# Kernel tuning notes

Hardware: AMD Instinct MI355X
Metric: run time of the kernel (lower is better)

Reference implementation:

```python
import jax, jax.numpy as jnp
import numpy as np
import math

H, W = 128, 128
FOV_X = 60.0
OPACITY_SCALE = 1.0
T_STOP = 1e-3  # early-termination threshold from the source (transmittance.max() < 0.001)
N_GAUSS = 2048


def setup_inputs() -> dict:
    key = jax.random.key(0)
    ks = jax.random.split(key, 6)
    N = N_GAUSS
    # place Gaussians in front of the camera so they rasterize (view_matrix = identity)
    xy = jax.random.uniform(ks[0], (N, 2), minval=-1.5, maxval=1.5, dtype=jnp.float32)
    z = jax.random.uniform(ks[1], (N, 1), minval=2.0, maxval=6.0, dtype=jnp.float32)
    positions = jnp.concatenate([xy, z], axis=1)
    scales = jax.random.uniform(ks[2], (N, 3), minval=0.02, maxval=0.08, dtype=jnp.float32)
    rotations = jax.random.normal(ks[3], (N, 4), dtype=jnp.float32)
    colors = jax.random.uniform(ks[4], (N, 3), dtype=jnp.float32)
    opacities = jax.random.uniform(ks[5], (N,), dtype=jnp.float32) * 0.9
    view_matrix = jnp.eye(4, dtype=jnp.float32)
    return {"positions": positions, "scales": scales, "rotations": rotations,
            "colors": colors, "opacities": opacities, "view_matrix": view_matrix}


def _preprocess(positions, scales, rotations, view_matrix):
    # quaternion (w,x,y,z) -> rotation matrix, same entry layout as the torch source
    q = rotations / (jnp.linalg.norm(rotations, axis=1, keepdims=True) + 1e-8)
    w, x, y, z = q[:, 0], q[:, 1], q[:, 2], q[:, 3]
    r00 = 1 - 2 * (y * y + z * z); r01 = 2 * (x * y + z * w); r02 = 2 * (x * z - y * w)
    r10 = 2 * (x * y - z * w); r11 = 1 - 2 * (x * x + z * z); r12 = 2 * (y * z + x * w)
    r20 = 2 * (x * z + y * w); r21 = 2 * (y * z - x * w); r22 = 1 - 2 * (x * x + y * y)
    Rm = jnp.stack([jnp.stack([r00, r01, r02], -1),
                    jnp.stack([r10, r11, r12], -1),
                    jnp.stack([r20, r21, r22], -1)], 1)  # (N,3,3)
    s2 = jnp.maximum(scales, 1e-6) ** 2
    # cov3d[i,k] = sum_j R[i,j] * s2[j] * R[k,j]
    cov3d = jnp.einsum('nij,nj,nkj->nik', Rm, s2, Rm)

    Rv = view_matrix[:3, :3]; tv = view_matrix[:3, 3]
    pos_cam = positions @ Rv.T + tv[None, :]
    X, Y, Z = pos_cam[:, 0], pos_cam[:, 1], pos_cam[:, 2]
    depths = Z
    valid = (Z > 0.1).astype(jnp.float32)

    fx = W / 2 / math.tan(math.radians(FOV_X) / 2)
    fy = fx
    Zs = jnp.maximum(Z, 1e-6)
    means_2d = jnp.stack([fx * X / Zs + W / 2, fy * Y / Zs + H / 2], 1)

    # projection Jacobian rows (N,3)
    invZ2 = 1.0 / Zs ** 2
    zeros = jnp.zeros_like(Zs)
    J0 = jnp.stack([fx / Zs, zeros, -fx * X * invZ2], 1)
    J1 = jnp.stack([zeros, fy / Zs, -fy * Y * invZ2], 1)
    SRt0 = jnp.einsum('nij,j->ni', cov3d, Rv[0])
    SRt1 = jnp.einsum('nij,j->ni', cov3d, Rv[1])
    c00 = jnp.sum(J0 * SRt0, 1)
    c01 = jnp.sum(J0 * SRt1, 1)
    c11 = jnp.sum(J1 * SRt1, 1)

    # radii from eigenvalue BEFORE the 1e-6 eye regularization (as in source)
    tr = c00 + c11
    det = c00 * c11 - c01 ** 2
    disc = jnp.maximum(tr ** 2 - 4 * det, 0.0)
    lam = (tr + jnp.sqrt(disc)) / 2.0
    radii = 3.0 * jnp.sqrt(jnp.maximum(lam, 1e-8))
    c00 = c00 + 1e-6
    c11 = c11 + 1e-6
    return means_2d, c00, c01, c11, depths, radii, valid


def _render(means_2d, c00, c01, c11, colors, opacities, depths, radii):
    # depth sort descending, exactly as torch.argsort(depths, descending=True)
    order = jnp.argsort(-depths)
    mu = means_2d[order]; col = colors[order]; op = opacities[order]; r = radii[order]
    c00 = c00[order]; c01 = c01[order]; c11 = c11[order]
    det = c00 * c11 - c01 ** 2 + 1e-8
    ic00 = (c11 / det)[:, None, None]
    ic01 = (-c01 / det)[:, None, None]
    ic11 = (c00 / det)[:, None, None]

    px = jnp.arange(W, dtype=jnp.float32)[None, None, :]   # (1,1,W)
    py = jnp.arange(H, dtype=jnp.float32)[None, :, None]   # (1,H,1)
    mux = mu[:, 0][:, None, None]; muy = mu[:, 1][:, None, None]
    rb = r[:, None, None]
    # bbox via int() truncation semantics of the source
    px_min = jnp.maximum(0.0, jnp.trunc(mux - rb)); px_max = jnp.minimum(float(W), jnp.trunc(mux + rb) + 1)
    py_min = jnp.maximum(0.0, jnp.trunc(muy - rb)); py_max = jnp.minimum(float(H), jnp.trunc(muy + rb) + 1)
    mask = (px >= px_min) & (px < px_max) & (py >= py_min) & (py < py_max)  # (N,H,W)

    dx = px - mux; dy = py - muy
    expo = -0.5 * (ic00 * dx * dx + 2 * ic01 * dx * dy + ic11 * dy * dy)
    G = jnp.exp(jnp.minimum(expo, 0.0))
    alpha = op[:, None, None] * G * mask  # (N,H,W), zero outside bbox (matching 'continue')

    # front-to-back transmittance product: T_i = prod_{j<i} (1 - alpha_j)
    T = jnp.cumprod(1.0 - alpha, axis=0)
    T_excl = jnp.concatenate([jnp.ones((1, H, W), alpha.dtype), T[:-1]], axis=0)
    # emulate the early break: splats processed only while max T >= 1e-3 (monotone)
    active = (jnp.max(T_excl, axis=(1, 2)) >= T_STOP).astype(alpha.dtype)
    weight = alpha * T_excl * active[:, None, None]
    image = jnp.einsum('nhw,nc->hwc', weight, col)  # (H,W,3)
    return image


def reference(positions, scales, rotations, colors, opacities, view_matrix):
    means_2d, c00, c01, c11, depths, radii, valid = _preprocess(positions, scales, rotations, view_matrix)
    op = opacities * OPACITY_SCALE * valid
    return _render(means_2d, c00, c01, c11, colors, op, depths, radii)
```

## Files before the change

### kernel.cpp

```cpp
#include <hip/hip_runtime.h>
#include <math.h>

#define NG 2048
#define WIMG 128
#define HIMG 128
#define SEG 16
#define RTILE 8
#define NTHREADS 1024

__device__ __forceinline__ void project_gaussian(
    const float* __restrict__ pos, const float* __restrict__ scales,
    const float* __restrict__ rot, const float* __restrict__ opac,
    const float* __restrict__ view, int i,
    float& depth, float& mux, float& muy,
    float& ic00, float& ic01, float& ic11,
    float& opv, unsigned& bbox)
{
    float qw = rot[4*i+0], qx = rot[4*i+1], qy = rot[4*i+2], qz = rot[4*i+3];
    float nrm = sqrtf(qw*qw + qx*qx + qy*qy + qz*qz) + 1e-8f;
    qw /= nrm; qx /= nrm; qy /= nrm; qz /= nrm;
    float R[3][3];
    R[0][0] = 1.f - 2.f*(qy*qy + qz*qz); R[0][1] = 2.f*(qx*qy + qz*qw); R[0][2] = 2.f*(qx*qz - qy*qw);
    R[1][0] = 2.f*(qx*qy - qz*qw); R[1][1] = 1.f - 2.f*(qx*qx + qz*qz); R[1][2] = 2.f*(qy*qz + qx*qw);
    R[2][0] = 2.f*(qx*qz + qy*qw); R[2][1] = 2.f*(qy*qz - qx*qw); R[2][2] = 1.f - 2.f*(qx*qx + qy*qy);

    float sv[3];
    sv[0] = fmaxf(scales[3*i+0], 1e-6f); sv[0] *= sv[0];
    sv[1] = fmaxf(scales[3*i+1], 1e-6f); sv[1] *= sv[1];
    sv[2] = fmaxf(scales[3*i+2], 1e-6f); sv[2] *= sv[2];

    float C[3][3];
    #pragma unroll
    for (int a = 0; a < 3; ++a)
        #pragma unroll
        for (int b = 0; b < 3; ++b)
            C[a][b] = R[a][0]*sv[0]*R[b][0] + R[a][1]*sv[1]*R[b][1] + R[a][2]*sv[2]*R[b][2];

    float Rv[3][3], tv[3];
    #pragma unroll
    for (int r = 0; r < 3; ++r) {
        Rv[r][0] = view[4*r+0]; Rv[r][1] = view[4*r+1]; Rv[r][2] = view[4*r+2];
        tv[r] = view[4*r+3];
    }
    float Px = pos[3*i], Py = pos[3*i+1], Pz = pos[3*i+2];
    float X = Rv[0][0]*Px + Rv[0][1]*Py + Rv[0][2]*Pz + tv[0];
    float Y = Rv[1][0]*Px + Rv[1][1]*Py + Rv[1][2]*Pz + tv[1];
    float Z = Rv[2][0]*Px + Rv[2][1]*Py + Rv[2][2]*Pz + tv[2];
    depth = Z;

    float valid = (Z > 0.1f) ? 1.f : 0.f;
    float Zs = fmaxf(Z, 1e-6f);
    const float fx = 110.85125168440814f;
    mux = fx * X / Zs + 64.f;
    muy = fx * Y / Zs + 64.f;
    float invZ2 = 1.f / (Zs * Zs);
    float J0[3] = { fx / Zs, 0.f, -fx * X * invZ2 };
    float J1[3] = { 0.f, fx / Zs, -fx * Y * invZ2 };

    float SRt0[3], SRt1[3];
    #pragma unroll
    for (int a = 0; a < 3; ++a) {
        SRt0[a] = C[a][0]*Rv[0][0] + C[a][1]*Rv[0][1] + C[a][2]*Rv[0][2];
        SRt1[a] = C[a][0]*Rv[1][0] + C[a][1]*Rv[1][1] + C[a][2]*Rv[1][2];
    }
    float c00 = J0[0]*SRt0[0] + J0[1]*SRt0[1] + J0[2]*SRt0[2];
    float c01 = J0[0]*SRt1[0] + J0[1]*SRt1[1] + J0[2]*SRt1[2];
    float c11 = J1[0]*SRt1[0] + J1[1]*SRt1[1] + J1[2]*SRt1[2];

    float trc = c00 + c11;
    float det = c00 * c11 - c01 * c01;
    float disc = fmaxf(trc*trc - 4.f*det, 0.f);
    float lam = 0.5f * (trc + sqrtf(disc));
    float rad = 3.f * sqrtf(fmaxf(lam, 1e-8f));
    c00 += 1e-6f; c11 += 1e-6f;
    float det2 = c00 * c11 - c01 * c01 + 1e-8f;
    ic00 = c11 / det2; ic01 = -c01 / det2; ic11 = c00 / det2;
    opv = opac[i] * valid;

    float pxmin = fmaxf(0.f,   truncf(mux - rad));
    float pxmax = fminf(128.f, truncf(mux + rad) + 1.f);
    float pymin = fmaxf(0.f,   truncf(muy - rad));
    float pymax = fminf(128.f, truncf(muy + rad) + 1.f);
    int ixmin = (int)fminf(pxmin, 255.f);
    int ixmax = (int)fmaxf(pxmax, 0.f);
    int iymin = (int)fminf(pymin, 255.f);
    int iymax = (int)fmaxf(pymax, 0.f);
    bbox = (unsigned)ixmin | ((unsigned)ixmax << 8)
         | ((unsigned)iymin << 16) | ((unsigned)iymax << 24);
}

__global__ void __launch_bounds__(NTHREADS)
tile_kernel(const float* __restrict__ pos,
            const float* __restrict__ scales,
            const float* __restrict__ rot,
            const float* __restrict__ colors,
            const float* __restrict__ opac,
            const float* __restrict__ view,
            float* __restrict__ out,
            int N)
{
    __shared__ int   hidx[NG];
    __shared__ float hdep[NG];
    __shared__ int   sidx[NG];
    __shared__ float4 part[SEG][64];
    __shared__ int   hcount;

    const int t = threadIdx.x;
    const int wid = t >> 6, lane = t & 63;
    const int tilesX = WIMG / RTILE;
    const int tileX = blockIdx.x % tilesX;
    const int tileY = blockIdx.x / tilesX;
    const int tx0 = tileX * RTILE, tx1 = tx0 + RTILE;
    const int ty0 = tileY * RTILE, ty1 = ty0 + RTILE;

    if (t == 0) hcount = 0;
    __syncthreads();

    for (int gb = 0; gb < N; gb += NTHREADS) {
        const int g = gb + t;
        bool hit = false;
        float depth = 0.f;
        if (g < N) {
            float mux, muy, i00, i01, i11, opv; unsigned bb;
            project_gaussian(pos, scales, rot, opac, view, g,
                             depth, mux, muy, i00, i01, i11, opv, bb);
            int xmin = bb & 255, xmax = (bb >> 8) & 255;
            int ymin = (bb >> 16) & 255, ymax = bb >> 24;
            hit = (xmin < tx1) && (xmax > tx0) && (ymin < ty1) && (ymax > ty0);
        }
        unsigned long long m = __ballot(hit);
        int cnt = __popcll(m);
        int base = 0;
        if (lane == 0) base = atomicAdd(&hcount, cnt);
        base = __shfl(base, 0);
        if (hit) {
            int off = __popcll(m & ((1ull << lane) - 1ull));
            hidx[base + off] = g;
            hdep[base + off] = depth;
        }
    }
    __syncthreads();
    const int K = hcount;

    for (int h = t; h < K; h += NTHREADS) {
        const float dh = hdep[h];
        const int   ih = hidx[h];
        int r = 0;
        for (int j = 0; j < K; ++j) {
            float dj = hdep[j];
            r += (dj > dh) || (dj == dh && hidx[j] < ih);
        }
        sidx[r] = ih;
    }
    __syncthreads();

    const int x = tx0 + (lane & (RTILE - 1));
    const int y = ty0 + (lane / RTILE);
    const float fpx = (float)x, fpy = (float)y;

    const int chunk = (K + SEG - 1) / SEG;
    const int k0 = wid * chunk;
    const int k1 = min(k0 + chunk, K);

    float T = 1.f, aR = 0.f, aG = 0.f, aB = 0.f;

    for (int base = k0; base < k1; base += 64) {
        const int cnt = min(64, k1 - base);
        float mux = 0.f, muy = 0.f, i00 = 0.f, i01 = 0.f, i11 = 0.f, opv = 0.f;
        float c0 = 0.f, c1 = 0.f, c2 = 0.f, depth;
        unsigned bb = 0;
        if (lane < cnt) {
            const int g = sidx[base + lane];
            project_gaussian(pos, scales, rot, opac, view, g,
                             depth, mux, muy, i00, i01, i11, opv, bb);
            c0 = colors[3*g+0]; c1 = colors[3*g+1]; c2 = colors[3*g+2];
        }
        for (int b = 0; b < cnt; ++b) {
            float bmux = __shfl(mux, b), bmuy = __shfl(muy, b);
            float b00 = __shfl(i00, b), b01 = __shfl(i01, b), b11 = __shfl(i11, b);
            float bop = __shfl(opv, b);
            float bc0 = __shfl(c0, b), bc1 = __shfl(c1, b), bc2 = __shfl(c2, b);
            unsigned bbb = __shfl(bb, b);
            int xmin = bbb & 255, xmax = (bbb >> 8) & 255;
            int ymin = (bbb >> 16) & 255, ymax = bbb >> 24;
            bool inside = (x >= xmin) && (x < xmax) && (y >= ymin) && (y < ymax);
            float dx = fpx - bmux, dy = fpy - bmuy;
            float e = -0.5f * (b00*dx*dx + 2.f*b01*dx*dy + b11*dy*dy);
            float G = __expf(fminf(e, 0.f));
            float alpha = inside ? (bop * G) : 0.f;
            float w = alpha * T;
            aR += w * bc0;
            aG += w * bc1;
            aB += w * bc2;
            T *= (1.f - alpha);
        }
    }

    part[wid][lane] = make_float4(aR, aG, aB, T);
    __syncthreads();

    if (t < 64) {
        float accR = 0.f, accG = 0.f, accB = 0.f, Tacc = 1.f;
        #pragma unroll
        for (int s = 0; s < SEG; ++s) {
            float4 p = part[s][t];
            accR += Tacc * p.x;
            accG += Tacc * p.y;
            accB += Tacc * p.z;
            Tacc *= p.w;
        }
        int xx = tx0 + (t & (RTILE - 1));
        int yy = ty0 + (t / RTILE);
        int idx = (yy * WIMG + xx) * 3;
        out[idx+0] = accR;
        out[idx+1] = accG;
        out[idx+2] = accB;
    }
}

extern "C" void kernel_launch(void* const* d_in, const int* in_sizes, int n_in,
                              void* d_out, int out_size, void* d_ws, size_t ws_size,
                              hipStream_t stream) {
    const float* pos    = (const float*)d_in[0];
    const float* scales = (const float*)d_in[1];
    const float* rot    = (const float*)d_in[2];
    const float* colors = (const float*)d_in[3];
    const float* opac   = (const float*)d_in[4];
    const float* view   = (const float*)d_in[5];
    float* out = (float*)d_out;
    const int N = in_sizes[4];

    const int nTiles = (WIMG / RTILE) * (HIMG / RTILE);
    tile_kernel<<<nTiles, NTHREADS, 0, stream>>>(
        pos, scales, rot, colors, opac, view, out, N);
}
```

Baseline: 19.18 us.

## Use cheap conservative bbox cull and warp-parallel rank sort per tile

The tile-binning pass no longer runs full Gaussian projection (quaternion normalisation, covariance, inverse). It uses a cheap conservative radius bound built from the largest scale and the Jacobian norm, and skips Gaussians behind the near plane. The O(K^2) rank sort now gives each warp one element and splits the comparison loop across lanes, followed by a shuffle reduction, instead of one thread scanning all K. The looser bound may let extra Gaussians into a tile. The render loop still applies the exact bbox test, so output should be unchanged if the bound is truly conservative.

```diff
diff --git a/kernel.cpp b/kernel.cpp
--- a/kernel.cpp
+++ b/kernel.cpp
@@ -99,11 +99,11 @@
             float* __restrict__ out,
             int N)
 {
-    __shared__ int   hidx[NG];
-    __shared__ float hdep[NG];
-    __shared__ int   sidx[NG];
+    __shared__ int    hidx[NG];
+    __shared__ float  hdep[NG];
+    __shared__ int    sidx[NG];
     __shared__ float4 part[SEG][64];
-    __shared__ int   hcount;
+    __shared__ int    hcount;
 
     const int t = threadIdx.x;
     const int wid = t >> 6, lane = t & 63;
@@ -116,17 +116,33 @@
     if (t == 0) hcount = 0;
     __syncthreads();
 
+    const float fx = 110.85125168440814f;
+    const float v00 = view[0], v01 = view[1],  v02 = view[2],  v03 = view[3];
+    const float v10 = view[4], v11 = view[5],  v12 = view[6],  v13 = view[7];
+    const float v20 = view[8], v21 = view[9],  v22 = view[10], v23 = view[11];
+
     for (int gb = 0; gb < N; gb += NTHREADS) {
         const int g = gb + t;
         bool hit = false;
-        float depth = 0.f;
+        float Z = 0.f;
         if (g < N) {
-            float mux, muy, i00, i01, i11, opv; unsigned bb;
-            project_gaussian(pos, scales, rot, opac, view, g,
-                             depth, mux, muy, i00, i01, i11, opv, bb);
-            int xmin = bb & 255, xmax = (bb >> 8) & 255;
-            int ymin = (bb >> 16) & 255, ymax = bb >> 24;
-            hit = (xmin < tx1) && (xmax > tx0) && (ymin < ty1) && (ymax > ty0);
+            float Px = pos[3*g], Py = pos[3*g+1], Pz = pos[3*g+2];
+            Z = v20*Px + v21*Py + v22*Pz + v23;
+            if (Z > 0.1f) {
+                float X = v00*Px + v01*Py + v02*Pz + v03;
+                float Y = v10*Px + v11*Py + v12*Pz + v13;
+                float invZ = 1.f / Z;
+                float mux = fx * X * invZ + 64.f;
+                float muy = fx * Y * invZ + 64.f;
+                float a = fx * invZ;
+                float b = -fx * X * invZ * invZ;
+                float c = -fx * Y * invZ * invZ;
+                float s0 = scales[3*g], s1 = scales[3*g+1], s2 = scales[3*g+2];
+                float smax = fmaxf(fmaxf(fmaxf(s0, s1), s2), 1e-6f);
+                float rbar = 3.f * smax * sqrtf(2.f*a*a + b*b + c*c) * 1.05f + 3.2e-4f;
+                hit = (mux - rbar < (float)tx1 + 1.f) && (mux + rbar > (float)tx0 - 1.f)
+                   && (muy - rbar < (float)ty1 + 1.f) && (muy + rbar > (float)ty0 - 1.f);
+            }
         }
         unsigned long long m = __ballot(hit);
         int cnt = __popcll(m);
@@ -136,21 +152,23 @@
         if (hit) {
             int off = __popcll(m & ((1ull << lane) - 1ull));
             hidx[base + off] = g;
-            hdep[base + off] = depth;
+            hdep[base + off] = Z;
         }
     }
     __syncthreads();
     const int K = hcount;
 
-    for (int h = t; h < K; h += NTHREADS) {
+    for (int h = wid; h < K; h += SEG) {
         const float dh = hdep[h];
         const int   ih = hidx[h];
         int r = 0;
-        for (int j = 0; j < K; ++j) {
+        for (int j = lane; j < K; j += 64) {
             float dj = hdep[j];
             r += (dj > dh) || (dj == dh && hidx[j] < ih);
         }
-        sidx[r] = ih;
+        #pragma unroll
+        for (int off = 32; off; off >>= 1) r += __shfl_xor(r, off);
+        if (lane == 0) sidx[r] = ih;
     }
     __syncthreads();
 
```

After: 25.36 us. +32.2%, slower.
